# Performance work log

Measured on AMD Instinct MI355X. Metric: run time of the kernel, lower is better.

## Reference

```python
import jax, jax.numpy as jnp
import numpy as np

N_NODES = 100000
N_EDGES = 3200000
D_IN = 256
D_OUT = 256


def setup_inputs() -> dict:
    key = jax.random.key(0)
    k1, k2, k3, k4, k5 = jax.random.split(key, 5)
    x = jax.random.normal(k1, (N_NODES, D_IN), dtype=jnp.float32)
    W = jax.random.normal(k2, (D_OUT, D_IN), dtype=jnp.float32) * (1.0 / np.sqrt(D_IN))
    edge_val = jax.random.uniform(k3, (N_EDGES,), dtype=jnp.float32)
    edge_row = jax.random.randint(k4, (N_EDGES,), 0, N_NODES, dtype=jnp.int32)
    edge_col = jax.random.randint(k5, (N_EDGES,), 0, N_NODES, dtype=jnp.int32)
    return {"x": x, "W": W, "edge_val": edge_val, "edge_row": edge_row, "edge_col": edge_col}


def reference(x, W, edge_val, edge_row, edge_col):
    # Linear (no bias): [N, D_in] @ [D_in, D_out] -> [N, D_out]
    h = x @ W.T
    # SpMM: out[r] = sum_e val[e] * h[col[e]] for edges with row[e] == r
    msgs = h[edge_col] * edge_val[:, None]          # [E, D_out] gather + scale
    out = jax.ops.segment_sum(msgs, edge_row, num_segments=N_NODES)  # scatter-add
    return out
```

## Files before the change

### kernel.cpp

```cpp
#include <hip/hip_runtime.h>
#include <hip/hip_bf16.h>

typedef float  f32x4 __attribute__((ext_vector_type(4)));
typedef short  s16x8 __attribute__((ext_vector_type(8)));
typedef unsigned short u16x8 __attribute__((ext_vector_type(8)));

#define N_NODES 100000
#define N_EDGES 3200000
#define DD 256

#define ROWS_PER_BKT 128
#define NBKT 782
#define BKT_CAP 4608
#define ACHUNK 3072
#define NABLK 1042
#define EDGES_PER_THREAD 12

#define BM 64
#define BN 256
#define BK 64
#define LDA 72
#define GEMM_BLOCKS 1563
#define NPAD (GEMM_BLOCKS * BM)
#define QSTRIDE 272

__device__ __forceinline__ ushort f2bf(float f) {
    union { __hip_bfloat16 b; ushort u; } cv;
    cv.b = __float2bfloat16(f);
    return cv.u;
}

__global__ __launch_bounds__(256) void wconv_kernel(const float* __restrict__ w, ushort* __restrict__ wb)
{
    int gid = blockIdx.x * 256 + threadIdx.x;
    float4 a = ((const float4*)w)[gid * 2];
    float4 b = ((const float4*)w)[gid * 2 + 1];
    u16x8 o = { f2bf(a.x), f2bf(a.y), f2bf(a.z), f2bf(a.w),
                f2bf(b.x), f2bf(b.y), f2bf(b.z), f2bf(b.w) };
    ((u16x8*)wb)[gid] = o;
}

__global__ __launch_bounds__(256) void gemm_q_kernel(
    const float* __restrict__ x, const ushort* __restrict__ wb,
    unsigned char* __restrict__ h8, float* __restrict__ hscale)
{
    __shared__ char smem[BM * LDA * 2 + BN * LDA * 2];
    ushort (*xs)[LDA]  = (ushort(*)[LDA])smem;
    ushort (*wsx)[LDA] = (ushort(*)[LDA])(smem + BM * LDA * 2);
    const int tid  = threadIdx.x;
    const int lane = tid & 63;
    const int wq   = tid >> 6;
    const int bm   = blockIdx.x * BM;
    const int l15 = lane & 15;
    const int lhi = lane >> 4;
    f32x4 acc[4][4] = {};

    for (int k0 = 0; k0 < DD; k0 += BK) {
        #pragma unroll
        for (int it = 0; it < 4; ++it) {
            int f = (it * 256 + tid) * 4;
            int r = f >> 6, c = f & 63;
            float4 v = make_float4(0.f, 0.f, 0.f, 0.f);
            if (bm + r < N_NODES) v = *(const float4*)(x + (size_t)(bm + r) * DD + k0 + c);
            *(ushort4*)&xs[r][c] = make_ushort4(f2bf(v.x), f2bf(v.y), f2bf(v.z), f2bf(v.w));
        }
        #pragma unroll
        for (int it = 0; it < 8; ++it) {
            int f = (it * 256 + tid) * 8;
            int r = f >> 6, c = f & 63;
            *(uint4*)&wsx[r][c] = *(const uint4*)(wb + (size_t)r * DD + k0 + c);
        }
        __syncthreads();
        #pragma unroll
        for (int kk = 0; kk < 2; ++kk) {
            const int koff = kk * 32 + lhi * 8;
            s16x8 a[4], b[4];
            #pragma unroll
            for (int m = 0; m < 4; ++m)
                a[m] = *(const s16x8*)&xs[m * 16 + l15][koff];
            #pragma unroll
            for (int n = 0; n < 4; ++n)
                b[n] = *(const s16x8*)&wsx[wq * 64 + n * 16 + l15][koff];
            #pragma unroll
            for (int m = 0; m < 4; ++m)
                #pragma unroll
                for (int n = 0; n < 4; ++n)
                    acc[m][n] = __builtin_amdgcn_mfma_f32_16x16x32_bf16(a[m], b[n], acc[m][n], 0, 0, 0);
        }
        __syncthreads();
    }

    float* wmax = (float*)smem;
    unsigned char* i8buf = (unsigned char*)(smem + 1024);

    float pmax[4][4];
    #pragma unroll
    for (int m = 0; m < 4; ++m)
        #pragma unroll
        for (int r = 0; r < 4; ++r)
            pmax[m][r] = fmaxf(fmaxf(fabsf(acc[m][0][r]), fabsf(acc[m][1][r])),
                               fmaxf(fabsf(acc[m][2][r]), fabsf(acc[m][3][r])));
    #pragma unroll
    for (int s = 1; s < 16; s <<= 1)
        #pragma unroll
        for (int m = 0; m < 4; ++m)
            #pragma unroll
            for (int r = 0; r < 4; ++r)
                pmax[m][r] = fmaxf(pmax[m][r], __shfl_xor(pmax[m][r], s));
    if (l15 == 0) {
        #pragma unroll
        for (int m = 0; m < 4; ++m)
            #pragma unroll
            for (int r = 0; r < 4; ++r)
                wmax[(m * 16 + lhi * 4 + r) * 4 + wq] = pmax[m][r];
    }
    __syncthreads();
    #pragma unroll
    for (int m = 0; m < 4; ++m)
        #pragma unroll
        for (int r = 0; r < 4; ++r) {
            const int R = m * 16 + lhi * 4 + r;
            f32x4 wv = *(const f32x4*)&wmax[R * 4];
            float rmax = fmaxf(fmaxf(fmaxf(wv[0], wv[1]), fmaxf(wv[2], wv[3])), 1e-30f);
            const float sc = 127.0f * __builtin_amdgcn_rcpf(rmax);
            #pragma unroll
            for (int n = 0; n < 4; ++n) {
                int q = (int)rintf(acc[m][n][r] * sc);
                i8buf[R * QSTRIDE + wq * 64 + n * 16 + l15] = (unsigned char)q;
            }
            if (wq == 0 && l15 == 0)
                hscale[bm + R] = rmax * (1.0f / 127.0f);
        }
    __syncthreads();
    #pragma unroll
    for (int it = 0; it < 4; ++it) {
        int idx = it * 256 + tid;
        int R = idx >> 4, w = idx & 15;
        *(uint4*)(h8 + (size_t)bm * 256 + (size_t)idx * 16) =
            *(const uint4*)&i8buf[R * QSTRIDE + w * 16];
    }
}

__global__ __launch_bounds__(256) void passA_kernel(
    const int* __restrict__ erow, const int* __restrict__ ecol,
    const float* __restrict__ eval, int* __restrict__ gcur,
    int2* __restrict__ pairsA)
{
    __shared__ int hist[NBKT];
    __shared__ int sbase[NBKT];
    __shared__ int scur[NBKT];
    __shared__ int rbase[NBKT];
    __shared__ int gsum[256];
    __shared__ int2 staged[ACHUNK];
    __shared__ int gdst[ACHUNK];
    const int tid = threadIdx.x;
    for (int i = tid; i < NBKT; i += 256) hist[i] = 0;
    __syncthreads();
    const int base = blockIdx.x * ACHUNK;
    int pk[EDGES_PER_THREAD]; float vv[EDGES_PER_THREAD]; int bk[EDGES_PER_THREAD];
    #pragma unroll
    for (int k = 0; k < EDGES_PER_THREAD; ++k) {
        int i = base + k * 256 + tid;
        bk[k] = -1;
        if (i < N_EDGES) {
            int r = erow[i];
            bk[k] = r >> 7;
            pk[k] = ecol[i] | ((r & 127) << 17);
            vv[k] = eval[i];
            atomicAdd(&hist[bk[k]], 1);
        }
    }
    __syncthreads();
    int gs = 0, lv[4];
    #pragma unroll
    for (int j = 0; j < 4; ++j) {
        int b = tid * 4 + j;
        lv[j] = (b < NBKT) ? hist[b] : 0;
        gs += lv[j];
    }
    gsum[tid] = gs;
    __syncthreads();
    for (int s = 1; s < 256; s <<= 1) {
        int t = (tid >= s) ? gsum[tid - s] : 0;
        __syncthreads();
        gsum[tid] += t;
        __syncthreads();
    }
    int run = gsum[tid] - gs;
    #pragma unroll
    for (int j = 0; j < 4; ++j) {
        int b = tid * 4 + j;
        if (b < NBKT) { sbase[b] = run; scur[b] = run; }
        run += lv[j];
    }
    __syncthreads();
    for (int b = tid; b < NBKT; b += 256) {
        int c = hist[b];
        if (c) rbase[b] = atomicAdd(&gcur[b], c);
    }
    __syncthreads();
    #pragma unroll
    for (int k = 0; k < EDGES_PER_THREAD; ++k) {
        if (bk[k] >= 0) {
            int lo = atomicAdd(&scur[bk[k]], 1);
            staged[lo] = make_int2(pk[k], __float_as_int(vv[k]));
            gdst[lo] = bk[k] * BKT_CAP + rbase[bk[k]] + (lo - sbase[bk[k]]);
        }
    }
    __syncthreads();
    const int cnt = min(ACHUNK, N_EDGES - base);
    for (int t = tid; t < cnt; t += 256)
        pairsA[gdst[t]] = staged[t];
}

__global__ __launch_bounds__(256) void passB_kernel(
    const int2* __restrict__ pairsA, const int* __restrict__ gcur,
    int2* __restrict__ pairsB, int2* __restrict__ row_se)
{
    __shared__ int hist[ROWS_PER_BKT];
    __shared__ int lds[ROWS_PER_BKT];
    __shared__ int cur[ROWS_PER_BKT];
    const int tid = threadIdx.x;
    const int b = blockIdx.x;
    const int cnt = gcur[b];
    const int base = b * BKT_CAP;
    if (tid < ROWS_PER_BKT) hist[tid] = 0;
    __syncthreads();
    for (int i = tid; i < cnt; i += 256)
        atomicAdd(&hist[(pairsA[base + i].x >> 17) & 127], 1);
    __syncthreads();
    int v = (tid < ROWS_PER_BKT) ? hist[tid] : 0;
    if (tid < ROWS_PER_BKT) lds[tid] = v;
    __syncthreads();
    for (int st = 1; st < ROWS_PER_BKT; st <<= 1) {
        int t = (tid >= st && tid < ROWS_PER_BKT) ? lds[tid - st] : 0;
        __syncthreads();
        if (tid < ROWS_PER_BKT) lds[tid] += t;
        __syncthreads();
    }
    if (tid < ROWS_PER_BKT) {
        int excl = lds[tid] - v;
        int r = b * ROWS_PER_BKT + tid;
        if (r < N_NODES) row_se[r] = make_int2(base + excl, base + excl + v);
        cur[tid] = base + excl;
    }
    __syncthreads();
    for (int i = tid; i < cnt; i += 256) {
        int2 p = pairsA[base + i];
        int rl = (p.x >> 17) & 127;
        int d = atomicAdd(&cur[rl], 1);
        pairsB[d] = make_int2(p.x & 0x1FFFF, p.y);
    }
}

__global__ __launch_bounds__(256) void spmm_kernel(
    const unsigned char* __restrict__ h8, const float* __restrict__ hscale,
    const int2* __restrict__ pairs, const int2* __restrict__ row_se,
    float* __restrict__ out)
{
    const int wid  = blockIdx.x * 4 + (threadIdx.x >> 6);
    const int lane = threadIdx.x & 63;
    if (wid >= N_NODES) return;
    const int2 se = row_se[wid];
    const int s = __builtin_amdgcn_readfirstlane(se.x);
    const int e = __builtin_amdgcn_readfirstlane(se.y);
    const int loff = lane * 4;
    float ax = 0.f, ay = 0.f, az = 0.f, aw = 0.f;

    int j = s;
    for (; j + 8 <= e; j += 8) {
        const int4* p4 = (const int4*)(pairs + j);
        int4 q0 = p4[0], q1 = p4[1], q2 = p4[2], q3 = p4[3];
        int   c[8] = { q0.x, q0.z, q1.x, q1.z, q2.x, q2.z, q3.x, q3.z };
        float v[8] = { __int_as_float(q0.y), __int_as_float(q0.w),
                       __int_as_float(q1.y), __int_as_float(q1.w),
                       __int_as_float(q2.y), __int_as_float(q2.w),
                       __int_as_float(q3.y), __int_as_float(q3.w) };
        float vs[8];
        #pragma unroll
        for (int t = 0; t < 8; ++t) vs[t] = v[t] * hscale[c[t]];
        unsigned hv[8];
        #pragma unroll
        for (int t = 0; t < 8; ++t)
            hv[t] = *(const unsigned*)(h8 + (size_t)c[t] * DD + loff);
        #pragma unroll
        for (int t = 0; t < 8; ++t) {
            ax += vs[t] * (float)((int)(hv[t] << 24) >> 24);
            ay += vs[t] * (float)((int)(hv[t] << 16) >> 24);
            az += vs[t] * (float)((int)(hv[t] <<  8) >> 24);
            aw += vs[t] * (float)((int)hv[t] >> 24);
        }
    }
    for (; j < e; ++j) {
        int2 p = pairs[j];
        const float vs = __int_as_float(p.y) * hscale[p.x];
        const unsigned hv = *(const unsigned*)(h8 + (size_t)p.x * DD + loff);
        ax += vs * (float)((int)(hv << 24) >> 24);
        ay += vs * (float)((int)(hv << 16) >> 24);
        az += vs * (float)((int)(hv <<  8) >> 24);
        aw += vs * (float)((int)hv >> 24);
    }
    f32x4 o = { ax, ay, az, aw };
    __builtin_nontemporal_store(o, (f32x4*)(out + (size_t)wid * DD + loff));
}

extern "C" void kernel_launch(void* const* d_in, const int* in_sizes, int n_in,
                              void* d_out, int out_size, void* d_ws, size_t ws_size,
                              hipStream_t stream)
{
    const float* x        = (const float*)d_in[0];
    const float* W        = (const float*)d_in[1];
    const float* edge_val = (const float*)d_in[2];
    const int*   edge_row = (const int*)d_in[3];
    const int*   edge_col = (const int*)d_in[4];
    float* out = (float*)d_out;

    char* ws = (char*)d_ws;
    size_t off = 0;
    auto alloc = [&](size_t bytes) {
        void* p = ws + off;
        off = (off + bytes + 255) & ~(size_t)255;
        return p;
    };
    unsigned char* h8     = (unsigned char*)alloc((size_t)NPAD * DD);
    float*         hscale = (float*)        alloc((size_t)NPAD * sizeof(float));
    int2*          pairsA = (int2*)alloc((size_t)NBKT * BKT_CAP * sizeof(int2));
    int2*          pairsB = (int2*)alloc((size_t)NBKT * BKT_CAP * sizeof(int2));
    ushort*        wb     = (ushort*)alloc((size_t)DD * DD * sizeof(ushort));
    int*           gcur   = (int*)alloc((size_t)NBKT * sizeof(int));
    int2*          row_se = (int2*)alloc((size_t)N_NODES * sizeof(int2));
    (void)ws_size;

    (void)hipMemsetAsync(gcur, 0, (size_t)NBKT * sizeof(int), stream);

    wconv_kernel<<<DD * DD / 8 / 256, 256, 0, stream>>>(W, wb);

    gemm_q_kernel<<<GEMM_BLOCKS, 256, 0, stream>>>(x, wb, h8, hscale);

    passA_kernel<<<NABLK, 256, 0, stream>>>(edge_row, edge_col, edge_val, gcur, pairsA);

    passB_kernel<<<NBKT, 256, 0, stream>>>(pairsA, gcur, pairsB, row_se);

    int spmm_blocks = (N_NODES + 3) / 4;
    spmm_kernel<<<spmm_blocks, 256, 0, stream>>>(h8, hscale, pairsB, row_se, out);
}
```

Baseline: 263.5 us.

## Load GEMM operands directly into MFMA registers and permute int8 h column layout

The GEMM kernel no longer stages x and W tiles through LDS. Each lane loads its MFMA operand fragments straight from global memory, converts x to bf16 in registers, and drops the per-tile barriers. The int8 output is written as packed 4-byte words in a permuted column order, removing the LDS transpose buffer. The SpMM kernel undoes that permutation through a small LDS buffer before its store. This trades LDS traffic and syncs for uncoalesced, redundant global loads of x and W, and adds an LDS shuffle in the SpMM epilogue.

```diff
diff --git a/kernel.cpp b/kernel.cpp
--- a/kernel.cpp
+++ b/kernel.cpp
@@ -16,13 +16,7 @@
 #define NABLK 1042
 #define EDGES_PER_THREAD 12
 
-#define BM 64
-#define BN 256
-#define BK 64
-#define LDA 72
 #define GEMM_BLOCKS 1563
-#define NPAD (GEMM_BLOCKS * BM)
-#define QSTRIDE 272
 
 __device__ __forceinline__ ushort f2bf(float f) {
     union { __hip_bfloat16 b; ushort u; } cv;
@@ -44,54 +38,46 @@
     const float* __restrict__ x, const ushort* __restrict__ wb,
     unsigned char* __restrict__ h8, float* __restrict__ hscale)
 {
-    __shared__ char smem[BM * LDA * 2 + BN * LDA * 2];
-    ushort (*xs)[LDA]  = (ushort(*)[LDA])smem;
-    ushort (*wsx)[LDA] = (ushort(*)[LDA])(smem + BM * LDA * 2);
+    __shared__ float wmax[64 * 4];
     const int tid  = threadIdx.x;
     const int lane = tid & 63;
     const int wq   = tid >> 6;
-    const int bm   = blockIdx.x * BM;
-    const int l15 = lane & 15;
-    const int lhi = lane >> 4;
+    const int bm   = blockIdx.x * 64;
+    const int l15  = lane & 15;
+    const int lhi  = lane >> 4;
     f32x4 acc[4][4] = {};
 
-    for (int k0 = 0; k0 < DD; k0 += BK) {
-        #pragma unroll
-        for (int it = 0; it < 4; ++it) {
-            int f = (it * 256 + tid) * 4;
-            int r = f >> 6, c = f & 63;
-            float4 v = make_float4(0.f, 0.f, 0.f, 0.f);
-            if (bm + r < N_NODES) v = *(const float4*)(x + (size_t)(bm + r) * DD + k0 + c);
-            *(ushort4*)&xs[r][c] = make_ushort4(f2bf(v.x), f2bf(v.y), f2bf(v.z), f2bf(v.w));
-        }
-        #pragma unroll
-        for (int it = 0; it < 8; ++it) {
-            int f = (it * 256 + tid) * 8;
-            int r = f >> 6, c = f & 63;
-            *(uint4*)&wsx[r][c] = *(const uint4*)(wb + (size_t)r * DD + k0 + c);
-        }
-        __syncthreads();
-        #pragma unroll
-        for (int kk = 0; kk < 2; ++kk) {
-            const int koff = kk * 32 + lhi * 8;
-            s16x8 a[4], b[4];
-            #pragma unroll
-            for (int m = 0; m < 4; ++m)
-                a[m] = *(const s16x8*)&xs[m * 16 + l15][koff];
+    bool rowok[4];
+    #pragma unroll
+    for (int m = 0; m < 4; ++m) rowok[m] = (bm + m * 16 + l15) < N_NODES;
+
+    const float*  xbase = x  + (size_t)(bm + l15) * DD + lhi * 8;
+    const ushort* wbase = wb + (size_t)(wq * 64 + l15) * DD + lhi * 8;
+
+    #pragma unroll 2
+    for (int kk = 0; kk < 8; ++kk) {
+        s16x8 a[4], b[4];
+        #pragma unroll
+        for (int n = 0; n < 4; ++n)
+            b[n] = *(const s16x8*)(wbase + (size_t)(n * 16) * DD + kk * 32);
+        #pragma unroll
+        for (int m = 0; m < 4; ++m) {
+            float4 lo = make_float4(0.f, 0.f, 0.f, 0.f);
+            float4 hi = make_float4(0.f, 0.f, 0.f, 0.f);
+            if (rowok[m]) {
+                const float* p = xbase + (size_t)(m * 16) * DD + kk * 32;
+                lo = *(const float4*)p;
+                hi = *(const float4*)(p + 4);
+            }
+            a[m] = (s16x8){ (short)f2bf(lo.x), (short)f2bf(lo.y), (short)f2bf(lo.z), (short)f2bf(lo.w),
+                            (short)f2bf(hi.x), (short)f2bf(hi.y), (short)f2bf(hi.z), (short)f2bf(hi.w) };
+        }
+        #pragma unroll
+        for (int m = 0; m < 4; ++m)
             #pragma unroll
             for (int n = 0; n < 4; ++n)
-                b[n] = *(const s16x8*)&wsx[wq * 64 + n * 16 + l15][koff];
-            #pragma unroll
-            for (int m = 0; m < 4; ++m)
-                #pragma unroll
-                for (int n = 0; n < 4; ++n)
-                    acc[m][n] = __builtin_amdgcn_mfma_f32_16x16x32_bf16(a[m], b[n], acc[m][n], 0, 0, 0);
-        }
-        __syncthreads();
-    }
-
-    float* wmax = (float*)smem;
-    unsigned char* i8buf = (unsigned char*)(smem + 1024);
+                acc[m][n] = __builtin_amdgcn_mfma_f32_16x16x32_bf16(a[m], b[n], acc[m][n], 0, 0, 0);
+    }
 
     float pmax[4][4];
     #pragma unroll
@@ -120,25 +106,19 @@
         #pragma unroll
         for (int r = 0; r < 4; ++r) {
             const int R = m * 16 + lhi * 4 + r;
+            const int row = bm + R;
+            if (row >= N_NODES) continue;
             f32x4 wv = *(const f32x4*)&wmax[R * 4];
             float rmax = fmaxf(fmaxf(fmaxf(wv[0], wv[1]), fmaxf(wv[2], wv[3])), 1e-30f);
             const float sc = 127.0f * __builtin_amdgcn_rcpf(rmax);
-            #pragma unroll
-            for (int n = 0; n < 4; ++n) {
-                int q = (int)rintf(acc[m][n][r] * sc);
-                i8buf[R * QSTRIDE + wq * 64 + n * 16 + l15] = (unsigned char)q;
-            }
-            if (wq == 0 && l15 == 0)
-                hscale[bm + R] = rmax * (1.0f / 127.0f);
-        }
-    __syncthreads();
-    #pragma unroll
-    for (int it = 0; it < 4; ++it) {
-        int idx = it * 256 + tid;
-        int R = idx >> 4, w = idx & 15;
-        *(uint4*)(h8 + (size_t)bm * 256 + (size_t)idx * 16) =
-            *(const uint4*)&i8buf[R * QSTRIDE + w * 16];
-    }
+            int q0 = (int)rintf(acc[m][0][r] * sc);
+            int q1 = (int)rintf(acc[m][1][r] * sc);
+            int q2 = (int)rintf(acc[m][2][r] * sc);
+            int q3 = (int)rintf(acc[m][3][r] * sc);
+            unsigned pack = (q0 & 255) | ((q1 & 255) << 8) | ((q2 & 255) << 16) | ((unsigned)(q3 & 255) << 24);
+            *(unsigned*)(h8 + (size_t)row * DD + wq * 64 + l15 * 4) = pack;
+            if (wq == 0 && l15 == 0) hscale[row] = rmax * (1.0f / 127.0f);
+        }
 }
 
 __global__ __launch_bounds__(256) void passA_kernel(
@@ -258,13 +238,16 @@
     const int2* __restrict__ pairs, const int2* __restrict__ row_se,
     float* __restrict__ out)
 {
-    const int wid  = blockIdx.x * 4 + (threadIdx.x >> 6);
+    __shared__ float obuf[4][256];
+    const int wave = threadIdx.x >> 6;
+    const int wid  = blockIdx.x * 4 + wave;
     const int lane = threadIdx.x & 63;
     if (wid >= N_NODES) return;
     const int2 se = row_se[wid];
     const int s = __builtin_amdgcn_readfirstlane(se.x);
     const int e = __builtin_amdgcn_readfirstlane(se.y);
     const int loff = lane * 4;
+    const int colbase = (lane >> 4) * 64 + (lane & 15);
     float ax = 0.f, ay = 0.f, az = 0.f, aw = 0.f;
 
     int j = s;
@@ -300,7 +283,11 @@
         az += vs * (float)((int)(hv <<  8) >> 24);
         aw += vs * (float)((int)hv >> 24);
     }
-    f32x4 o = { ax, ay, az, aw };
+    obuf[wave][colbase +  0] = ax;
+    obuf[wave][colbase + 16] = ay;
+    obuf[wave][colbase + 32] = az;
+    obuf[wave][colbase + 48] = aw;
+    f32x4 o = *(const f32x4*)&obuf[wave][loff];
     __builtin_nontemporal_store(o, (f32x4*)(out + (size_t)wid * DD + loff));
 }
 
@@ -322,8 +309,8 @@
         off = (off + bytes + 255) & ~(size_t)255;
         return p;
     };
-    unsigned char* h8     = (unsigned char*)alloc((size_t)NPAD * DD);
-    float*         hscale = (float*)        alloc((size_t)NPAD * sizeof(float));
+    unsigned char* h8     = (unsigned char*)alloc((size_t)N_NODES * DD);
+    float*         hscale = (float*)alloc((size_t)N_NODES * sizeof(float));
     int2*          pairsA = (int2*)alloc((size_t)NBKT * BKT_CAP * sizeof(int2));
     int2*          pairsB = (int2*)alloc((size_t)NBKT * BKT_CAP * sizeof(int2));
     ushort*        wb     = (ushort*)alloc((size_t)DD * DD * sizeof(ushort));
```

Result: slower. 293.4 us (+11.4%).
